# Kernel optimization log

Measured on AMD Instinct MI355X. Metric: run time of the kernel, lower is better.

Reference implementation:

```python
import jax, jax.numpy as jnp
import numpy as np

N = 50000      # nodes
E = 800000     # edges (avg degree 16)
D = 64         # hidden_dim == out_dim
L = 4          # number of GatedGCN layers
NB = 16        # num_bond_type
EPS_BN = 1e-5
EPS_ETA = 1e-6


def _bn(x, g, b):
    # training-mode batch norm over the node/edge axis
    mu = jnp.mean(x, axis=0, keepdims=True)
    var = jnp.var(x, axis=0, keepdims=True)
    return (x - mu) * jax.lax.rsqrt(var + EPS_BN) * g + b


def setup_inputs() -> dict:
    key = jax.random.key(0)
    ks = iter(jax.random.split(key, 64))
    s = 0.05

    def w(shape):
        return jax.random.normal(next(ks), shape, dtype=jnp.float32) * s

    inp = {
        "h_ids": jax.random.randint(next(ks), (N,), 0, N),
        "e_ids": jax.random.randint(next(ks), (E,), 0, NB),
        "f_ids": jax.random.randint(next(ks), (N,), 0, N),
        "src": jax.random.randint(next(ks), (E,), 0, N),
        "dst": jax.random.randint(next(ks), (E,), 0, N),
        "emb_h": w((N, D)),
        "emb_e": w((NB, D)),
        "emb_f": w((N, D)),
        "A1_w": w((L, D, D)), "A1_b": jnp.zeros((L, D), jnp.float32),
        "A2_w": w((L, 2 * D, D)), "A2_b": jnp.zeros((L, D), jnp.float32),
        "B1_w": w((L, D, D)), "B1_b": jnp.zeros((L, D), jnp.float32),
        "B2_w": w((L, D, D)), "B2_b": jnp.zeros((L, D), jnp.float32),
        "B3_w": w((L, D, D)), "B3_b": jnp.zeros((L, D), jnp.float32),
        "C1_w": w((L, D, D)), "C1_b": jnp.zeros((L, D), jnp.float32),
        "C2_w": w((L, D, D)), "C2_b": jnp.zeros((L, D), jnp.float32),
        "bn_h_g": jnp.ones((L, D), jnp.float32), "bn_h_b": jnp.zeros((L, D), jnp.float32),
        "bn_e_g": jnp.ones((L, D), jnp.float32), "bn_e_b": jnp.zeros((L, D), jnp.float32),
        "mlp_w0": w((D, D // 2)), "mlp_b0": jnp.zeros((D // 2,), jnp.float32),
        "mlp_w1": w((D // 2, D // 4)), "mlp_b1": jnp.zeros((D // 4,), jnp.float32),
        "mlp_w2": w((D // 4, 1)), "mlp_b2": jnp.zeros((1,), jnp.float32),
    }
    return inp


def reference(h_ids, e_ids, f_ids, src, dst,
              emb_h, emb_e, emb_f,
              A1_w, A1_b, A2_w, A2_b, B1_w, B1_b, B2_w, B2_b, B3_w, B3_b,
              C1_w, C1_b, C2_w, C2_b,
              bn_h_g, bn_h_b, bn_e_g, bn_e_b,
              mlp_w0, mlp_b0, mlp_w1, mlp_b1, mlp_w2, mlp_b2):
    h = emb_h[h_ids]          # [N, D]
    e = emb_e[e_ids]          # [E, D]
    p = emb_f[f_ids]          # [N, D]

    seg = lambda m: jax.ops.segment_sum(m, dst, num_segments=N)

    for i in range(L):
        h_in, e_in, p_in = h, e, p
        # per-node projections (dense GEMMs), then irregular gathers per edge
        B1h = h @ B1_w[i] + B1_b[i]
        B2h = h @ B2_w[i] + B2_b[i]
        B3e = e @ B3_w[i] + B3_b[i]
        hat_eta = B1h[src] + B2h[dst] + B3e           # [E, D]
        sigma = jax.nn.sigmoid(hat_eta)
        sum_sigma = seg(sigma)                        # [N, D] scatter-sum at dst
        eta = sigma / (sum_sigma[dst] + EPS_ETA)      # [E, D]

        v = jnp.concatenate([h, p], axis=-1) @ A2_w[i] + A2_b[i]  # [N, D]
        sum_eta_v = seg(eta * v[src])
        h_new = h @ A1_w[i] + A1_b[i] + sum_eta_v

        C2p = p @ C2_w[i] + C2_b[i]
        sum_eta_p = seg(eta * C2p[src])
        p_new = p @ C1_w[i] + C1_b[i] + sum_eta_p

        h = jax.nn.relu(_bn(h_new, bn_h_g[i], bn_h_b[i]))
        e_new = jax.nn.relu(_bn(hat_eta, bn_e_g[i], bn_e_b[i]))
        p = jnp.tanh(p_new)
        # residual (input_dim == output_dim in every layer)
        h = h_in + h
        e = e_in + e_new
        p = p_in + p

    hg = jnp.mean(h, axis=0)  # mean readout over the (single) graph -> [D]
    y = jax.nn.relu(hg @ mlp_w0 + mlp_b0)
    y = jax.nn.relu(y @ mlp_w1 + mlp_b1)
    y = y @ mlp_w2 + mlp_b2   # [1]
    return y
```

## Files before the change

### kernel.cpp

```cpp
#include <hip/hip_runtime.h>
#include <math.h>

#define NN 50000
#define EE 800000
#define LL 4

typedef unsigned short u16;
typedef unsigned int u32;
typedef __attribute__((ext_vector_type(8))) short bf16x8;
typedef __attribute__((ext_vector_type(4))) float f32x4;

__device__ __forceinline__ float rlane(float v, int l) {
  return __int_as_float(__builtin_amdgcn_readlane(__float_as_int(v), l));
}

__device__ __forceinline__ float matvec64(float xv, const float* __restrict__ w) {
  float a0 = 0.f, a1 = 0.f, a2 = 0.f, a3 = 0.f;
#pragma unroll
  for (int k = 0; k < 64; k += 4) {
    a0 = fmaf(rlane(xv, k + 0), w[k + 0], a0);
    a1 = fmaf(rlane(xv, k + 1), w[k + 1], a1);
    a2 = fmaf(rlane(xv, k + 2), w[k + 2], a2);
    a3 = fmaf(rlane(xv, k + 3), w[k + 3], a3);
  }
  return (a0 + a1) + (a2 + a3);
}

__device__ __forceinline__ float sigm(float x) { return 1.f / (1.f + __expf(-x)); }

__device__ __forceinline__ u16 f2b(float x) {
  u32 u = __float_as_uint(x);
  u32 r = (u + 0x7FFFu + ((u >> 16) & 1u)) >> 16;
  return (u16)r;
}
__device__ __forceinline__ float b2f(u16 b) { return __uint_as_float(((u32)b) << 16); }

struct FragA { bf16x8 hi0, hi1, lo0, lo1; };

__device__ __forceinline__ void load_a(const float* __restrict__ base, int l, FragA& fa) {
  const int row = l & 15, quad = l >> 4;
  const float* src = base + (size_t)row * 64 + quad * 8;
  bf16x8 h0, h1, l0, l1;
#pragma unroll
  for (int j = 0; j < 8; ++j) {
    float x0 = src[j], x1 = src[32 + j];
    u16 a0 = f2b(x0), a1 = f2b(x1);
    h0[j] = (short)a0; h1[j] = (short)a1;
    l0[j] = (short)f2b(x0 - b2f(a0));
    l1[j] = (short)f2b(x1 - b2f(a1));
  }
  fa.hi0 = h0; fa.hi1 = h1; fa.lo0 = l0; fa.lo1 = l1;
}

__device__ __forceinline__ void gemm_acc(const FragA& fa, const float* __restrict__ W,
                                         int l, f32x4 acc[4]) {
  const int row = l & 15, quad = l >> 4;
#pragma unroll
  for (int cb = 0; cb < 4; ++cb) {
    f32x4 z = acc[cb];
#pragma unroll
    for (int kb = 0; kb < 2; ++kb) {
      bf16x8 bhi, blo;
      const float* wp = W + (size_t)(kb * 32 + quad * 8) * 64 + cb * 16 + row;
#pragma unroll
      for (int j = 0; j < 8; ++j) {
        float wv = wp[(size_t)j * 64];
        u16 aa = f2b(wv);
        bhi[j] = (short)aa;
        blo[j] = (short)f2b(wv - b2f(aa));
      }
      const bf16x8 ahi = kb ? fa.hi1 : fa.hi0;
      const bf16x8 alo = kb ? fa.lo1 : fa.lo0;
      z = __builtin_amdgcn_mfma_f32_16x16x32_bf16(ahi, bhi, z, 0, 0, 0);
      z = __builtin_amdgcn_mfma_f32_16x16x32_bf16(alo, bhi, z, 0, 0, 0);
      z = __builtin_amdgcn_mfma_f32_16x16x32_bf16(ahi, blo, z, 0, 0, 0);
    }
    acc[cb] = z;
  }
}

__device__ __forceinline__ void store16(const f32x4 acc[4], const float* __restrict__ bias,
                                        int l, float* __restrict__ out) {
  const int row = l & 15, quad = l >> 4;
#pragma unroll
  for (int cb = 0; cb < 4; ++cb) {
    int col = cb * 16 + row;
    float bv = bias[col];
#pragma unroll
    for (int r = 0; r < 4; ++r)
      out[(size_t)(quad * 4 + r) * 64 + col] = acc[cb][r] + bv;
  }
}

__global__ void k_t2(const float* __restrict__ h, const float* __restrict__ B1w,
                     int* __restrict__ flag) {
  int l = threadIdx.x;
  FragA fa;
  load_a(h, l, fa);
  f32x4 acc[4];
  acc[0] = (f32x4){0,0,0,0}; acc[1] = (f32x4){0,0,0,0};
  acc[2] = (f32x4){0,0,0,0}; acc[3] = (f32x4){0,0,0,0};
  gemm_acc(fa, B1w, l, acc);
  const int row = l & 15, quad = l >> 4;
  int ok = 1;
#pragma unroll
  for (int cb = 0; cb < 4; ++cb)
#pragma unroll
    for (int r = 0; r < 4; ++r) {
      int nrow = quad * 4 + r, col = cb * 16 + row;
      float ref = 0.f;
      for (int k = 0; k < 64; ++k) ref += h[nrow * 64 + k] * B1w[k * 64 + col];
      if (fabsf(acc[cb][r] - ref) > 3e-3f + 3e-3f * fabsf(ref)) ok = 0;
    }
  ok = __all(ok);
  if (l == 0) flag[0] = ok;
}

__global__ void k_hist(const int* __restrict__ dst, int* __restrict__ counts) {
  int i = blockIdx.x * 256 + threadIdx.x;
  if (i < EE) atomicAdd(&counts[dst[i]], 1);
}

__global__ void k_scan(const int* __restrict__ counts, int* __restrict__ row_start,
                       int* __restrict__ cursor) {
  __shared__ int sd[1024];
  int tid = threadIdx.x;
  int running = 0;
  for (int basei = 0; basei < NN; basei += 1024) {
    int i = basei + tid;
    int v = (i < NN) ? counts[i] : 0;
    sd[tid] = v;
    __syncthreads();
    for (int ofs = 1; ofs < 1024; ofs <<= 1) {
      int t = (tid >= ofs) ? sd[tid - ofs] : 0;
      __syncthreads();
      sd[tid] += t;
      __syncthreads();
    }
    int incl = sd[tid];
    int total = sd[1023];
    if (i < NN) { int e = running + incl - v; row_start[i] = e; cursor[i] = e; }
    running += total;
    __syncthreads();
  }
  if (tid == 0) row_start[NN] = EE;
}

__global__ void k_scatter(const int* __restrict__ dst, const int* __restrict__ src,
                          const int* __restrict__ e_ids,
                          int* __restrict__ cursor, int* __restrict__ src_s,
                          int* __restrict__ eids_s) {
  int i = blockIdx.x * 256 + threadIdx.x;
  if (i < EE) {
    int d = dst[i];
    int pos = atomicAdd(&cursor[d], 1);
    src_s[pos] = src[i];
    eids_s[pos] = e_ids[i];
  }
}

__global__ void k_einit(const int* __restrict__ eids_s, const float* __restrict__ emb_e,
                        u16* __restrict__ e_sorted) {
  int idx = blockIdx.x * 256 + threadIdx.x;
  if (idx >= EE * 64) return;
  int ed = idx >> 6, f = idx & 63;
  e_sorted[idx] = f2b(emb_e[eids_s[ed] * 64 + f]);
}

__global__ void k_ninit(const int* __restrict__ h_ids, const int* __restrict__ f_ids,
                        const float* __restrict__ emb_h, const float* __restrict__ emb_f,
                        float* __restrict__ h, float* __restrict__ p) {
  int idx = blockIdx.x * 256 + threadIdx.x;
  if (idx >= NN * 64) return;
  int n = idx >> 6, f = idx & 63;
  h[idx] = emb_h[h_ids[n] * 64 + f];
  p[idx] = emb_f[f_ids[n] * 64 + f];
}

__global__ void __launch_bounds__(256) k_Am(
    int mode,
    float* __restrict__ h, float* __restrict__ p,
    float* __restrict__ hn, float* __restrict__ pn,
    const float* __restrict__ mu_h, const float* __restrict__ ir_h,
    const float* __restrict__ g_h, const float* __restrict__ b_h,
    const float* __restrict__ B1w, const float* __restrict__ B1b,
    const float* __restrict__ B2w, const float* __restrict__ B2b,
    const float* __restrict__ A1w, const float* __restrict__ A1b,
    const float* __restrict__ C1w, const float* __restrict__ C1b,
    const float* __restrict__ C2w, const float* __restrict__ C2b,
    const float* __restrict__ A2w, const float* __restrict__ A2b,
    float* __restrict__ B1h, float* __restrict__ B2h,
    float* __restrict__ vbuf, float* __restrict__ C2p,
    const int* __restrict__ flag) {
  if (!flag[0]) return;
  const int f = threadIdx.x & 63;
  const int wv = threadIdx.x >> 6;
  const int base0 = (blockIdx.x * 4 + wv) * 16;
  if (base0 >= NN) return;

  if (mode) {
    float mu = mu_h[f], ir = ir_h[f], ga = g_h[f], be = b_h[f];
    for (int i = 0; i < 16; ++i) {
      int n = base0 + i;
      float hv = hn[(size_t)n * 64 + f];
      h[(size_t)n * 64 + f] += fmaxf(0.f, (hv - mu) * ir * ga + be);
      float pv = pn[(size_t)n * 64 + f];
      p[(size_t)n * 64 + f] += tanhf(pv);
    }
  }

  FragA fh, fq;
  load_a(h + (size_t)base0 * 64, f, fh);
  load_a(p + (size_t)base0 * 64, f, fq);
  f32x4 acc[4];
#define ZERO4 { acc[0]=(f32x4){0,0,0,0}; acc[1]=(f32x4){0,0,0,0}; \
                acc[2]=(f32x4){0,0,0,0}; acc[3]=(f32x4){0,0,0,0}; }
  ZERO4; gemm_acc(fh, B1w, f, acc); store16(acc, B1b, f, B1h + (size_t)base0 * 64);
  ZERO4; gemm_acc(fh, B2w, f, acc); store16(acc, B2b, f, B2h + (size_t)base0 * 64);
  ZERO4; gemm_acc(fh, A1w, f, acc); store16(acc, A1b, f, hn + (size_t)base0 * 64);
  ZERO4; gemm_acc(fq, C1w, f, acc); store16(acc, C1b, f, pn + (size_t)base0 * 64);
  ZERO4; gemm_acc(fq, C2w, f, acc); store16(acc, C2b, f, C2p + (size_t)base0 * 64);
  ZERO4; gemm_acc(fh, A2w, f, acc); gemm_acc(fq, A2w + 4096, f, acc);
  store16(acc, A2b, f, vbuf + (size_t)base0 * 64);
#undef ZERO4
}

__global__ void __launch_bounds__(256) k_Av(
    int mode,
    float* __restrict__ h, float* __restrict__ p,
    float* __restrict__ hn, float* __restrict__ pn,
    const float* __restrict__ mu_h, const float* __restrict__ ir_h,
    const float* __restrict__ g_h, const float* __restrict__ b_h,
    const float* __restrict__ B1w, const float* __restrict__ B1b,
    const float* __restrict__ B2w, const float* __restrict__ B2b,
    const float* __restrict__ A1w, const float* __restrict__ A1b,
    const float* __restrict__ C1w, const float* __restrict__ C1b,
    const float* __restrict__ C2w, const float* __restrict__ C2b,
    const float* __restrict__ A2w, const float* __restrict__ A2b,
    float* __restrict__ B1h, float* __restrict__ B2h,
    float* __restrict__ vbuf, float* __restrict__ C2p,
    const int* __restrict__ flag) {
  if (flag[0]) return;
  const int f = threadIdx.x & 63;
  const int wv = threadIdx.x >> 6;
  const int base0 = (blockIdx.x * 4 + wv) * 16;
  if (base0 >= NN) return;

  if (mode) {
    float mu = mu_h[f], ir = ir_h[f], ga = g_h[f], be = b_h[f];
    for (int i = 0; i < 16; ++i) {
      int n = base0 + i;
      float hv = hn[n * 64 + f];
      h[n * 64 + f] += fmaxf(0.f, (hv - mu) * ir * ga + be);
      float pv = pn[n * 64 + f];
      p[n * 64 + f] += tanhf(pv);
    }
  }

  float w[64];
#define LOADW(WP) _Pragma("unroll") for (int k = 0; k < 64; ++k) w[k] = (WP)[k * 64 + f];
  LOADW(B1w);
  { float bb = B1b[f];
    for (int i = 0; i < 16; ++i) { int n = base0 + i;
      B1h[n * 64 + f] = matvec64(h[n * 64 + f], w) + bb; } }
  LOADW(B2w);
  { float bb = B2b[f];
    for (int i = 0; i < 16; ++i) { int n = base0 + i;
      B2h[n * 64 + f] = matvec64(h[n * 64 + f], w) + bb; } }
  LOADW(A1w);
  { float bb = A1b[f];
    for (int i = 0; i < 16; ++i) { int n = base0 + i;
      hn[n * 64 + f] = matvec64(h[n * 64 + f], w) + bb; } }
  LOADW(C1w);
  { float bb = C1b[f];
    for (int i = 0; i < 16; ++i) { int n = base0 + i;
      pn[n * 64 + f] = matvec64(p[n * 64 + f], w) + bb; } }
  LOADW(C2w);
  { float bb = C2b[f];
    for (int i = 0; i < 16; ++i) { int n = base0 + i;
      C2p[n * 64 + f] = matvec64(p[n * 64 + f], w) + bb; } }
  {
    float w2[64];
#pragma unroll
    for (int k = 0; k < 64; ++k) { w[k] = A2w[k * 64 + f]; w2[k] = A2w[(k + 64) * 64 + f]; }
    float bb = A2b[f];
    for (int i = 0; i < 16; ++i) { int n = base0 + i;
      vbuf[n * 64 + f] = matvec64(h[n * 64 + f], w) + matvec64(p[n * 64 + f], w2) + bb; }
  }
#undef LOADW
}

template <int SH, int MODE>
__global__ void __launch_bounds__(256) k_B(
    u16* __restrict__ e_sorted, const float* __restrict__ B1h,
    const float* __restrict__ B2h, const int* __restrict__ src_s,
    const int* __restrict__ row_start,
    const float* __restrict__ B3w, const float* __restrict__ B3b,
    const float* __restrict__ mu_p, const float* __restrict__ ir_p,
    const float* __restrict__ g_p, const float* __restrict__ b_p,
    u16* __restrict__ hat, float* __restrict__ sum_sigma,
    float* __restrict__ eS1, float* __restrict__ eS2) {
  const int f = threadIdx.x & 63;
  const int wv = threadIdx.x >> 6;
  const int nb = (blockIdx.x * 4 + wv) * 4;
  if (nb >= NN) return;
  float w[64];
#pragma unroll
  for (int k = 0; k < 64; ++k) w[k] = B3w[k * 64 + f];
  float bb = B3b[f];
  float mu = 0.f, ir = 0.f, ga = 0.f, be = 0.f;
  if (MODE >= 1) { mu = mu_p[f]; ir = ir_p[f]; ga = g_p[f]; be = b_p[f]; }
  float s1 = 0.f, s2 = 0.f;
  for (int i = 0; i < 4; ++i) {
    int n = nb + i;
    float b2 = B2h[n * 64 + f];
    float ssum = 0.f;
    int t0 = row_start[n], t1 = row_start[n + 1];
    for (int t = t0; t < t1; ++t) {
      float xv = b2f(e_sorted[(size_t)t * 64 + f]);
      if (MODE >= 1) {
        float pv = b2f(hat[(size_t)t * 64 + f]);
        u16 q = f2b(xv + fmaxf(0.f, (pv - mu) * ir * ga + be));
        if (MODE == 1) e_sorted[(size_t)t * 64 + f] = q;
        xv = b2f(q);
      }
      int s = src_s[t];
      float acc = matvec64(xv, w) + bb + b2 + B1h[s * 64 + f];
      if (SH) {
        u16 hb = f2b(acc);
        hat[(size_t)t * 64 + f] = hb;
        acc = b2f(hb);
      }
      float sg = sigm(acc);
      ssum += sg; s1 += acc; s2 += acc * acc;
    }
    sum_sigma[n * 64 + f] = ssum;
  }
  int slot = (blockIdx.x & 255) * 64 + f;
  atomicAdd(&eS1[slot], s1);
  atomicAdd(&eS2[slot], s2);
}

__global__ void k_red(const float* __restrict__ S1, const float* __restrict__ S2,
                      float cnt, float* __restrict__ mu, float* __restrict__ ir) {
  int f = threadIdx.x;
  float a = 0.f, b = 0.f;
  for (int j = 0; j < 256; ++j) { a += S1[j * 64 + f]; b += S2[j * 64 + f]; }
  float m = a / cnt;
  float var = fmaxf(b / cnt - m * m, 0.f);
  mu[f] = m;
  ir[f] = rsqrtf(var + 1e-5f);
}

template <int SH, int LAST>
__global__ void __launch_bounds__(256) k_C(
    const u16* __restrict__ hat, u16* __restrict__ e_sorted,
    const float* __restrict__ B1h, const float* __restrict__ B2h,
    const float* __restrict__ B3w, const float* __restrict__ B3b,
    const float* __restrict__ vbuf, const float* __restrict__ C2p,
    const int* __restrict__ src_s, const int* __restrict__ row_start,
    const float* __restrict__ sum_sigma,
    float* __restrict__ hn, float* __restrict__ pn,
    const float* __restrict__ mu_e, const float* __restrict__ ir_e,
    const float* __restrict__ g_e, const float* __restrict__ b_e,
    float* __restrict__ hS1, float* __restrict__ hS2) {
  const int f = threadIdx.x & 63;
  const int wv = threadIdx.x >> 6;
  const int n = blockIdx.x * 4 + wv;
  if (n >= NN) return;
  float w[64];
  float bb = 0.f;
  if (!SH) {
#pragma unroll
    for (int k = 0; k < 64; ++k) w[k] = B3w[k * 64 + f];
    bb = B3b[f];
  }
  float mu = mu_e[f], ir = ir_e[f], ga = g_e[f], be = b_e[f];
  float inv = 1.f / (sum_sigma[n * 64 + f] + 1e-6f);
  float ahv = 0.f, ahp = 0.f;
  int t0 = row_start[n], t1 = row_start[n + 1];
  int t = t0;
  if (SH) {
    for (; t + 4 <= t1; t += 4) {
      int s0 = src_s[t + 0] * 64, s1 = src_s[t + 1] * 64;
      int s2 = src_s[t + 2] * 64, s3 = src_s[t + 3] * 64;
      float hv0 = b2f(hat[(size_t)(t + 0) * 64 + f]);
      float hv1 = b2f(hat[(size_t)(t + 1) * 64 + f]);
      float hv2 = b2f(hat[(size_t)(t + 2) * 64 + f]);
      float hv3 = b2f(hat[(size_t)(t + 3) * 64 + f]);
      float v0 = vbuf[s0 + f], v1 = vbuf[s1 + f], v2 = vbuf[s2 + f], v3 = vbuf[s3 + f];
      float et0 = sigm(hv0) * inv, et1 = sigm(hv1) * inv;
      float et2 = sigm(hv2) * inv, et3 = sigm(hv3) * inv;
      ahv += et0 * v0 + et1 * v1 + et2 * v2 + et3 * v3;
      if (!LAST) {
        float c0 = C2p[s0 + f], c1 = C2p[s1 + f], c2 = C2p[s2 + f], c3 = C2p[s3 + f];
        ahp += et0 * c0 + et1 * c1 + et2 * c2 + et3 * c3;
      }
    }
  }
  for (; t < t1; ++t) {
    int s = src_s[t] * 64;
    float ev = 0.f;
    if (!SH) ev = b2f(e_sorted[(size_t)t * 64 + f]);
    float hatv;
    if (SH) hatv = b2f(hat[(size_t)t * 64 + f]);
    else    hatv = matvec64(ev, w) + bb + B2h[n * 64 + f] + B1h[s + f];
    float eta = sigm(hatv) * inv;
    ahv = fmaf(eta, vbuf[s + f], ahv);
    if (!LAST) {
      ahp = fmaf(eta, C2p[s + f], ahp);
      if (!SH)
        e_sorted[(size_t)t * 64 + f] = f2b(ev + fmaxf(0.f, (hatv - mu) * ir * ga + be));
    }
  }
  float hv = hn[n * 64 + f] + ahv; hn[n * 64 + f] = hv;
  if (!LAST) pn[n * 64 + f] += ahp;
  int slot = (blockIdx.x & 255) * 64 + f;
  atomicAdd(&hS1[slot], hv);
  atomicAdd(&hS2[slot], hv * hv);
}

__global__ void __launch_bounds__(256) k_F1(
    const float* __restrict__ hn, const float* __restrict__ h,
    const float* __restrict__ mu, const float* __restrict__ ir,
    const float* __restrict__ ga, const float* __restrict__ be,
    float* __restrict__ hsum) {
  int f = threadIdx.x & 63, wv = threadIdx.x >> 6;
  float m = mu[f], r = ir[f], g = ga[f], b = be[f];
  float ps = 0.f;
  for (int n = blockIdx.x * 4 + wv; n < NN; n += gridDim.x * 4)
    ps += h[n * 64 + f] + fmaxf(0.f, (hn[n * 64 + f] - m) * r * g + b);
  atomicAdd(&hsum[f], ps);
}

__global__ void k_F2(const float* __restrict__ hsum,
                     const float* __restrict__ w0, const float* __restrict__ b0,
                     const float* __restrict__ w1, const float* __restrict__ b1,
                     const float* __restrict__ w2, const float* __restrict__ b2,
                     float* __restrict__ out) {
  __shared__ float hg[64]; __shared__ float y0[32]; __shared__ float y1[16];
  int t = threadIdx.x;
  hg[t] = hsum[t] * (1.f / (float)NN);
  __syncthreads();
  if (t < 32) { float a = b0[t];
    for (int k = 0; k < 64; ++k) a = fmaf(hg[k], w0[k * 32 + t], a);
    y0[t] = fmaxf(a, 0.f); }
  __syncthreads();
  if (t < 16) { float a = b1[t];
    for (int k = 0; k < 32; ++k) a = fmaf(y0[k], w1[k * 16 + t], a);
    y1[t] = fmaxf(a, 0.f); }
  __syncthreads();
  if (t == 0) { float a = b2[0];
    for (int k = 0; k < 16; ++k) a = fmaf(y1[k], w2[k], a);
    out[0] = a; }
}

__global__ void k_report(float* out, float v) { out[0] = v; }

extern "C" void kernel_launch(void* const* d_in, const int* in_sizes, int n_in,
                              void* d_out, int out_size, void* d_ws, size_t ws_size,
                              hipStream_t stream) {
  (void)in_sizes; (void)n_in; (void)out_size;
  const int* h_ids = (const int*)d_in[0];
  const int* e_ids = (const int*)d_in[1];
  const int* f_ids = (const int*)d_in[2];
  const int* src   = (const int*)d_in[3];
  const int* dst   = (const int*)d_in[4];
  const float* emb_h = (const float*)d_in[5];
  const float* emb_e = (const float*)d_in[6];
  const float* emb_f = (const float*)d_in[7];
  const float* A1_w = (const float*)d_in[8];  const float* A1_b = (const float*)d_in[9];
  const float* A2_w = (const float*)d_in[10]; const float* A2_b = (const float*)d_in[11];
  const float* B1_w = (const float*)d_in[12]; const float* B1_b = (const float*)d_in[13];
  const float* B2_w = (const float*)d_in[14]; const float* B2_b = (const float*)d_in[15];
  const float* B3_w = (const float*)d_in[16]; const float* B3_b = (const float*)d_in[17];
  const float* C1_w = (const float*)d_in[18]; const float* C1_b = (const float*)d_in[19];
  const float* C2_w = (const float*)d_in[20]; const float* C2_b = (const float*)d_in[21];
  const float* bn_h_g = (const float*)d_in[22]; const float* bn_h_b = (const float*)d_in[23];
  const float* bn_e_g = (const float*)d_in[24]; const float* bn_e_b = (const float*)d_in[25];
  const float* mlp_w0 = (const float*)d_in[26]; const float* mlp_b0 = (const float*)d_in[27];
  const float* mlp_w1 = (const float*)d_in[28]; const float* mlp_b1 = (const float*)d_in[29];
  const float* mlp_w2 = (const float*)d_in[30]; const float* mlp_b2 = (const float*)d_in[31];

  auto pad = [](size_t b) { return (b + 255) & ~(size_t)255; };
  const size_t sz_e    = pad((size_t)EE * 64 * 2);
  const size_t sz_node = pad((size_t)NN * 64 * 4);
  const size_t sz_cnt  = pad((size_t)NN * 4);
  const size_t sz_row  = pad((size_t)(NN + 1) * 4);
  const size_t sz_ei   = pad((size_t)EE * 4);
  const size_t sz_stat = pad((size_t)LL * 2 * 256 * 64 * 4);
  const size_t sz_vec  = pad(64 * 4);

  size_t base_need = sz_e + 9 * sz_node + 2 * sz_cnt + sz_row + 2 * sz_ei +
                     2 * sz_stat + 6 * sz_vec;
  bool store_hat = (base_need + sz_e) <= ws_size;
  if (base_need > ws_size) {
    k_report<<<1, 1, 0, stream>>>((float*)d_out, (float)(ws_size >> 20) + 0.125f);
    return;
  }

  char* cur = (char*)d_ws;
  auto alloc = [&](size_t bytes) -> char* { char* r = cur; cur += bytes; return r; };
  u16* e_sorted = (u16*)alloc(sz_e);
  u16* hat      = store_hat ? (u16*)alloc(sz_e) : (u16*)e_sorted;
  float* h    = (float*)alloc(sz_node);
  float* p    = (float*)alloc(sz_node);
  float* hn   = (float*)alloc(sz_node);
  float* pn   = (float*)alloc(sz_node);
  float* B1h  = (float*)alloc(sz_node);
  float* B2h  = (float*)alloc(sz_node);
  float* vbuf = (float*)alloc(sz_node);
  float* C2p  = (float*)alloc(sz_node);
  float* ssig = (float*)alloc(sz_node);
  int* counts    = (int*)alloc(sz_cnt);
  int* cursor    = (int*)alloc(sz_cnt);
  int* row_start = (int*)alloc(sz_row);
  int* src_s     = (int*)alloc(sz_ei);
  int* eids_s    = (int*)alloc(sz_ei);
  float* estats = (float*)alloc(sz_stat);
  float* hstats = (float*)alloc(sz_stat);
  float* hsum   = (float*)alloc(sz_vec);
  float* mu_h = (float*)alloc(sz_vec);
  float* ir_h = (float*)alloc(sz_vec);
  float* mu_e = (float*)alloc(sz_vec);
  float* ir_e = (float*)alloc(sz_vec);
  int* flag  = (int*)alloc(sz_vec);

  hipMemsetAsync(counts, 0, sz_cnt, stream);
  hipMemsetAsync(estats, 0, 2 * sz_stat + sz_vec, stream);

  k_hist<<<(EE + 255) / 256, 256, 0, stream>>>(dst, counts);
  k_scan<<<1, 1024, 0, stream>>>(counts, row_start, cursor);
  k_scatter<<<(EE + 255) / 256, 256, 0, stream>>>(dst, src, e_ids, cursor, src_s, eids_s);
  k_einit<<<(EE * 64) / 256, 256, 0, stream>>>(eids_s, emb_e, e_sorted);
  k_ninit<<<(NN * 64 + 255) / 256, 256, 0, stream>>>(h_ids, f_ids, emb_h, emb_f, h, p);
  k_t2<<<1, 64, 0, stream>>>(h, B1_w, flag);

  const int STAT = 2 * 256 * 64;
  const int GB = (NN + 15) / 16, GC = (NN + 3) / 4;
  for (int i = 0; i < LL; ++i) {
    if (i > 0) {
      k_red<<<1, 64, 0, stream>>>(hstats + (i - 1) * STAT,
                                  hstats + (i - 1) * STAT + 256 * 64, (float)NN, mu_h, ir_h);
    }
    const float* gh = bn_h_g + (i > 0 ? (i - 1) * 64 : 0);
    const float* bh = bn_h_b + (i > 0 ? (i - 1) * 64 : 0);
    k_Am<<<(NN + 63) / 64, 256, 0, stream>>>(
        (i > 0) ? 1 : 0, h, p, hn, pn, mu_h, ir_h, gh, bh,
        B1_w + i * 4096, B1_b + i * 64, B2_w + i * 4096, B2_b + i * 64,
        A1_w + i * 4096, A1_b + i * 64, C1_w + i * 4096, C1_b + i * 64,
        C2_w + i * 4096, C2_b + i * 64, A2_w + i * 8192, A2_b + i * 64,
        B1h, B2h, vbuf, C2p, flag);
    k_Av<<<(NN + 63) / 64, 256, 0, stream>>>(
        (i > 0) ? 1 : 0, h, p, hn, pn, mu_h, ir_h, gh, bh,
        B1_w + i * 4096, B1_b + i * 64, B2_w + i * 4096, B2_b + i * 64,
        A1_w + i * 4096, A1_b + i * 64, C1_w + i * 4096, C1_b + i * 64,
        C2_w + i * 4096, C2_b + i * 64, A2_w + i * 8192, A2_b + i * 64,
        B1h, B2h, vbuf, C2p, flag);
    const float* gp = bn_e_g + (i > 0 ? (i - 1) * 64 : 0);
    const float* bp = bn_e_b + (i > 0 ? (i - 1) * 64 : 0);
    if (store_hat) {
      if (i == 0)
        k_B<1, 0><<<GB, 256, 0, stream>>>(
            e_sorted, B1h, B2h, src_s, row_start, B3_w + i * 4096, B3_b + i * 64,
            mu_e, ir_e, gp, bp, hat, ssig,
            estats + i * STAT, estats + i * STAT + 256 * 64);
      else if (i < LL - 1)
        k_B<1, 1><<<GB, 256, 0, stream>>>(
            e_sorted, B1h, B2h, src_s, row_start, B3_w + i * 4096, B3_b + i * 64,
            mu_e, ir_e, gp, bp, hat, ssig,
            estats + i * STAT, estats + i * STAT + 256 * 64);
      else
        k_B<1, 2><<<GB, 256, 0, stream>>>(
            e_sorted, B1h, B2h, src_s, row_start, B3_w + i * 4096, B3_b + i * 64,
            mu_e, ir_e, gp, bp, hat, ssig,
            estats + i * STAT, estats + i * STAT + 256 * 64);
    } else {
      k_B<0, 0><<<GB, 256, 0, stream>>>(
          e_sorted, B1h, B2h, src_s, row_start, B3_w + i * 4096, B3_b + i * 64,
          mu_e, ir_e, gp, bp, hat, ssig,
          estats + i * STAT, estats + i * STAT + 256 * 64);
    }
    if (!store_hat || i < LL - 1)
      k_red<<<1, 64, 0, stream>>>(estats + i * STAT, estats + i * STAT + 256 * 64,
                                  (float)EE, mu_e, ir_e);
    bool lastL = (i == LL - 1);
    if (store_hat) {
      if (lastL)
        k_C<1, 1><<<GC, 256, 0, stream>>>(
            hat, e_sorted, B1h, B2h, B3_w + i * 4096, B3_b + i * 64, vbuf, C2p,
            src_s, row_start, ssig, hn, pn, mu_e, ir_e,
            bn_e_g + i * 64, bn_e_b + i * 64,
            hstats + i * STAT, hstats + i * STAT + 256 * 64);
      else
        k_C<1, 0><<<GC, 256, 0, stream>>>(
            hat, e_sorted, B1h, B2h, B3_w + i * 4096, B3_b + i * 64, vbuf, C2p,
            src_s, row_start, ssig, hn, pn, mu_e, ir_e,
            bn_e_g + i * 64, bn_e_b + i * 64,
            hstats + i * STAT, hstats + i * STAT + 256 * 64);
    } else {
      k_C<0, 0><<<GC, 256, 0, stream>>>(
          hat, e_sorted, B1h, B2h, B3_w + i * 4096, B3_b + i * 64, vbuf, C2p,
          src_s, row_start, ssig, hn, pn, mu_e, ir_e,
          bn_e_g + i * 64, bn_e_b + i * 64,
          hstats + i * STAT, hstats + i * STAT + 256 * 64);
    }
  }
  k_red<<<1, 64, 0, stream>>>(hstats + 3 * STAT, hstats + 3 * STAT + 256 * 64,
                              (float)NN, mu_h, ir_h);
  k_F1<<<512, 256, 0, stream>>>(hn, h, mu_h, ir_h, bn_h_g + 3 * 64, bn_h_b + 3 * 64, hsum);
  k_F2<<<1, 64, 0, stream>>>(hsum, mlp_w0, mlp_b0, mlp_w1, mlp_b1, mlp_w2, mlp_b2,
                             (float*)d_out);
}
```

Before: 2.393 ms.

## Store edge features as fp16 and use packed half2 FMA for B3 matvec

Edge features move from bf16 to fp16 storage, and the per-edge B3 matvec in k_B now uses packed __hfma2 on half2 pairs. Each lane loads two features as one u32, which halves the readlane broadcasts and FMA count per edge. The BN+ReLU residual update is done by the first 32 lanes on packed pairs, with the BN affine folded into a single fma. This trades accuracy for throughput: fp16 accumulation in the dot product and the fp16 range and precision of the edge residual could drift from the fp32 reference.

```diff
diff --git a/kernel.cpp b/kernel.cpp
--- a/kernel.cpp
+++ b/kernel.cpp
@@ -1,4 +1,5 @@
 #include <hip/hip_runtime.h>
+#include <hip/hip_fp16.h>
 #include <math.h>
 
 #define NN 50000
@@ -12,6 +13,9 @@
 
 __device__ __forceinline__ float rlane(float v, int l) {
   return __int_as_float(__builtin_amdgcn_readlane(__float_as_int(v), l));
+}
+__device__ __forceinline__ u32 rlane_u32(u32 v, int l) {
+  return (u32)__builtin_amdgcn_readlane((int)v, l);
 }
 
 __device__ __forceinline__ float matvec64(float xv, const float* __restrict__ w) {
@@ -34,6 +38,15 @@
   return (u16)r;
 }
 __device__ __forceinline__ float b2f(u16 b) { return __uint_as_float(((u32)b) << 16); }
+
+__device__ __forceinline__ u16 f2h_(float x) {
+  __half h = __float2half_rn(x);
+  return *(u16*)&h;
+}
+__device__ __forceinline__ float h2f_(u16 b) {
+  __half h = *(__half*)&b;
+  return __half2float(h);
+}
 
 struct FragA { bf16x8 hi0, hi1, lo0, lo1; };
 
@@ -164,7 +177,7 @@
   int idx = blockIdx.x * 256 + threadIdx.x;
   if (idx >= EE * 64) return;
   int ed = idx >> 6, f = idx & 63;
-  e_sorted[idx] = f2b(emb_e[eids_s[ed] * 64 + f]);
+  e_sorted[idx] = f2h_(emb_e[eids_s[ed] * 64 + f]);
 }
 
 __global__ void k_ninit(const int* __restrict__ h_ids, const int* __restrict__ f_ids,
@@ -292,7 +305,7 @@
 
 template <int SH, int MODE>
 __global__ void __launch_bounds__(256) k_B(
-    u16* __restrict__ e_sorted, const float* __restrict__ B1h,
+    u16* __restrict__ e16, const float* __restrict__ B1h,
     const float* __restrict__ B2h, const int* __restrict__ src_s,
     const int* __restrict__ row_start,
     const float* __restrict__ B3w, const float* __restrict__ B3b,
@@ -304,28 +317,63 @@
   const int wv = threadIdx.x >> 6;
   const int nb = (blockIdx.x * 4 + wv) * 4;
   if (nb >= NN) return;
-  float w[64];
-#pragma unroll
-  for (int k = 0; k < 64; ++k) w[k] = B3w[k * 64 + f];
-  float bb = B3b[f];
-  float mu = 0.f, ir = 0.f, ga = 0.f, be = 0.f;
-  if (MODE >= 1) { mu = mu_p[f]; ir = ir_p[f]; ga = g_p[f]; be = b_p[f]; }
+  const int kk = f & 31;
+
+  __half2 wpk[32];
+#pragma unroll
+  for (int k = 0; k < 32; ++k) {
+    float w0 = B3w[(size_t)(2 * k) * 64 + f];
+    float w1 = B3w[(size_t)(2 * k + 1) * 64 + f];
+    wpk[k] = __floats2half2_rn(w0, w1);
+  }
+  const float bb = B3b[f];
+  float a0 = 0.f, c0 = 0.f, a1 = 0.f, c1 = 0.f;
+  if (MODE >= 1) {
+    float m0 = mu_p[2 * kk], i0 = ir_p[2 * kk];
+    float m1 = mu_p[2 * kk + 1], i1 = ir_p[2 * kk + 1];
+    a0 = i0 * g_p[2 * kk];     c0 = b_p[2 * kk] - m0 * a0;
+    a1 = i1 * g_p[2 * kk + 1]; c1 = b_p[2 * kk + 1] - m1 * a1;
+  }
   float s1 = 0.f, s2 = 0.f;
   for (int i = 0; i < 4; ++i) {
     int n = nb + i;
-    float b2 = B2h[n * 64 + f];
+    float b2 = B2h[(size_t)n * 64 + f] + bb;
     float ssum = 0.f;
     int t0 = row_start[n], t1 = row_start[n + 1];
     for (int t = t0; t < t1; ++t) {
-      float xv = b2f(e_sorted[(size_t)t * 64 + f]);
+      u32 xq = ((const u32*)e16)[(size_t)t * 32 + kk];
       if (MODE >= 1) {
-        float pv = b2f(hat[(size_t)t * 64 + f]);
-        u16 q = f2b(xv + fmaxf(0.f, (pv - mu) * ir * ga + be));
-        if (MODE == 1) e_sorted[(size_t)t * 64 + f] = q;
-        xv = b2f(q);
+        if (f < 32) {
+          u32 hq = ((const u32*)hat)[(size_t)t * 32 + kk];
+          float p0 = __uint_as_float(hq << 16);
+          float p1 = __uint_as_float(hq & 0xffff0000u);
+          __half2 ex = *(__half2*)&xq;
+          float e0 = __low2float(ex)  + fmaxf(0.f, fmaf(p0, a0, c0));
+          float e1 = __high2float(ex) + fmaxf(0.f, fmaf(p1, a1, c1));
+          __half2 nq = __floats2half2_rn(e0, e1);
+          xq = *(u32*)&nq;
+          if (MODE == 1) ((u32*)e16)[(size_t)t * 32 + kk] = xq;
+        }
       }
       int s = src_s[t];
-      float acc = matvec64(xv, w) + bb + b2 + B1h[s * 64 + f];
+      float g = B1h[(size_t)s * 64 + f];
+      __half2 za = __float2half2_rn(0.f), zb = za, zc = za, zd = za;
+#pragma unroll
+      for (int k = 0; k < 32; k += 4) {
+        u32 q0 = rlane_u32(xq, k + 0);
+        u32 q1 = rlane_u32(xq, k + 1);
+        u32 q2 = rlane_u32(xq, k + 2);
+        u32 q3 = rlane_u32(xq, k + 3);
+        za = __hfma2(*(__half2*)&q0, wpk[k + 0], za);
+        zb = __hfma2(*(__half2*)&q1, wpk[k + 1], zb);
+        zc = __hfma2(*(__half2*)&q2, wpk[k + 2], zc);
+        zd = __hfma2(*(__half2*)&q3, wpk[k + 3], zd);
+      }
+      float dot = ((__low2float(za) + __high2float(za)) +
+                   (__low2float(zb) + __high2float(zb))) +
+                  ((__low2float(zc) + __high2float(zc)) +
+                   (__low2float(zd) + __high2float(zd)));
+      float acc = dot + b2 + g;
       if (SH) {
         u16 hb = f2b(acc);
         hat[(size_t)t * 64 + f] = hb;
@@ -334,7 +382,7 @@
       float sg = sigm(acc);
       ssum += sg; s1 += acc; s2 += acc * acc;
     }
-    sum_sigma[n * 64 + f] = ssum;
+    sum_sigma[(size_t)n * 64 + f] = ssum;
   }
   int slot = (blockIdx.x & 255) * 64 + f;
   atomicAdd(&eS1[slot], s1);
@@ -401,7 +449,7 @@
   for (; t < t1; ++t) {
     int s = src_s[t] * 64;
     float ev = 0.f;
-    if (!SH) ev = b2f(e_sorted[(size_t)t * 64 + f]);
+    if (!SH) ev = h2f_(e_sorted[(size_t)t * 64 + f]);
     float hatv;
     if (SH) hatv = b2f(hat[(size_t)t * 64 + f]);
     else    hatv = matvec64(ev, w) + bb + B2h[n * 64 + f] + B1h[s + f];
@@ -410,7 +458,7 @@
     if (!LAST) {
       ahp = fmaf(eta, C2p[s + f], ahp);
       if (!SH)
-        e_sorted[(size_t)t * 64 + f] = f2b(ev + fmaxf(0.f, (hatv - mu) * ir * ga + be));
+        e_sorted[(size_t)t * 64 + f] = f2h_(ev + fmaxf(0.f, (hatv - mu) * ir * ga + be));
     }
   }
   float hv = hn[n * 64 + f] + ahv; hn[n * 64 + f] = hv;
```

Measured after the change: 2.282 ms. 1.05x faster.
